# Performance work log

Hardware: AMD Instinct MI355X
Metric: run time of the kernel (lower is better)

Reference implementation:

```python
import jax, jax.numpy as jnp
import numpy as np

B, T, D, H, MLP, NI, OUT = 256, 2049, 64, 64, 128, 128, 10
L = D + D * (D - 1) // 2  # depth-2 logsignature channels = 2080


def _logsig_depth2(X, n_intervals):
    """Depth-2 log-signature of a piecewise-linear path over equal intervals.
    X: [B, T, D] with T = n_intervals*s + 1. Returns [B, n_intervals, L] where
    L = D + D(D-1)/2 (level-1 increments + strictly-upper-triangular Levy areas,
    the Lyndon-word basis signatory uses at depth 2)."""
    Bq, Tq, Dq = X.shape
    s = (Tq - 1) // n_intervals
    idx = np.arange(n_intervals)[:, None] * s + np.arange(s + 1)[None, :]
    seg = X[:, idx]                       # [B, n, s+1, D]
    inc = seg[:, :, -1] - seg[:, :, 0]    # level 1: [B, n, D]
    dlt = seg[:, :, 1:] - seg[:, :, :-1]  # per-step increments [B, n, s, D]
    cum = seg[:, :, :-1] - seg[:, :, :1]  # partial increments  [B, n, s, D]
    M = jnp.einsum('bnki,bnkj->bnij', cum, dlt)
    A = 0.5 * (M - jnp.swapaxes(M, -1, -2))  # Levy area [B, n, D, D]
    iu, ju = np.triu_indices(Dq, 1)
    return jnp.concatenate([inc, A[..., iu, ju]], axis=-1)  # [B, n, L]


def setup_inputs() -> dict:
    key = jax.random.key(0)
    ks = jax.random.split(key, 10)
    X = jax.random.normal(ks[0], (B, T, D), jnp.float32) * 0.05
    W_in = jax.random.normal(ks[1], (D, H), jnp.float32) / np.sqrt(D)
    b_in = jnp.zeros((H,), jnp.float32)
    W1 = jax.random.normal(ks[2], (H, MLP), jnp.float32) / np.sqrt(H)
    b1 = jnp.zeros((MLP,), jnp.float32)
    W2 = jax.random.normal(ks[3], (MLP, D * L), jnp.float32) / np.sqrt(MLP)
    b2 = jnp.zeros((D * L,), jnp.float32)
    W_out = jax.random.normal(ks[4], (H, OUT), jnp.float32) / np.sqrt(H)
    b_out = jnp.zeros((OUT,), jnp.float32)
    return {"X": X, "W_in": W_in, "b_in": b_in, "W1": W1, "b1": b1,
            "W2": W2, "b2": b2, "W_out": W_out, "b_out": b_out,
            "n_intervals": NI}


def reference(X, W_in, b_in, W1, b1, W2, b2, W_out, b_out, n_intervals):
    Bq, Tq, Dq = X.shape
    logsig = _logsig_depth2(X, n_intervals)        # [B, n, L]
    h0 = X[:, 0] @ W_in + b_in                     # initial_linear

    def vf(h):  # F.forward: MLP(h) -> [B, D, L]
        z = jnp.tanh(h @ W1 + b1)
        return (z @ W2 + b2).reshape(Bq, Dq, -1)

    def g(h, ls):  # f(h) contracted with logsig derivative
        return jnp.einsum('bdl,bl->bd', vf(h), ls)

    def rk4_step(h, ls):  # one RK4 step per interval, dt = 1
        k1 = g(h, ls)
        k2 = g(h + 0.5 * k1, ls)
        k3 = g(h + 0.5 * k2, ls)
        k4 = g(h + k3, ls)
        return h + (k1 + 2.0 * k2 + 2.0 * k3 + k4) / 6.0, None

    hT, _ = jax.lax.scan(rk4_step, h0, jnp.swapaxes(logsig, 0, 1))
    return hT @ W_out + b_out  # readout_linear: [B, OUT]
```

## Files before the change

### kernel.cpp

```cpp
#include <hip/hip_runtime.h>
#include <hip/hip_bf16.h>
#include <cstdint>
#include <cstddef>

#define B_SZ   256
#define T_SZ   2049
#define D_SZ   64
#define H_SZ   64
#define MLP_SZ 128
#define NI_SZ  128
#define SEG    16
#define KDIM   2080
#define KP     2112
#define OUT_SZ 10

#define NC     32
#define NCHUNK (NI_SZ / NC)
#define MROWS  (NC * B_SZ)
#define NB     8448
#define GSTR   8256
#define NT     (KP / 64)

typedef _Float16 f16x8 __attribute__((ext_vector_type(8)));
typedef float    f32x4 __attribute__((ext_vector_type(4)));

__device__ __forceinline__ float rlane(float v, int l) {
    return __uint_as_float(__builtin_amdgcn_readlane(__float_as_uint(v), l));
}

__global__ __launch_bounds__(256) void build_B(const float* __restrict__ W2,
                                               const float* __restrict__ b2,
                                               _Float16* __restrict__ Bm) {
    const int r = blockIdx.x, t = threadIdx.x;
    const float* src = nullptr;
    if (r < 8192) {
        const int d = r >> 7, m = r & 127;
        src = W2 + (size_t)m * (64 * KDIM) + (size_t)d * KDIM;
    } else if (r < 8256) {
        src = b2 + (size_t)(r - 8192) * KDIM;
    }
    _Float16* dst = Bm + (size_t)r * KP;
    for (int l = t; l < KP; l += 256)
        dst[l] = (src && l < KDIM) ? (_Float16)src[l] : (_Float16)0.0f;
}

__global__ void h0_kernel(const float* __restrict__ X, const float* __restrict__ W_in,
                          const float* __restrict__ b_in, float* __restrict__ h_state) {
    const int b = blockIdx.x, t = threadIdx.x;
    __shared__ float x0[D_SZ];
    if (t < D_SZ) x0[t] = X[(size_t)b * T_SZ * D_SZ + t];
    __syncthreads();
    float acc = b_in[t];
    for (int k = 0; k < D_SZ; ++k) acc += x0[k] * W_in[k * H_SZ + t];
    h_state[b * H_SZ + t] = acc;
}

__global__ __launch_bounds__(256) void logsig_kernel(const float* __restrict__ X,
                                                     _Float16* __restrict__ LS,
                                                     int n0) {
    const int b = blockIdx.x, sl = blockIdx.y, t = threadIdx.x;
    const int n = n0 + sl;
    __shared__ float seg[SEG + 1][D_SZ];
    __shared__ float cum[SEG][D_SZ];
    __shared__ float dlt[SEG][D_SZ];
    __shared__ float Mm[D_SZ][D_SZ + 1];

    const float* Xp = X + ((size_t)b * T_SZ + (size_t)n * SEG) * D_SZ;
    for (int i = t; i < (SEG + 1) * D_SZ / 4; i += 256)
        ((float4*)&seg[0][0])[i] = ((const float4*)Xp)[i];
    __syncthreads();
    for (int i = t; i < SEG * D_SZ; i += 256) {
        const int k = i >> 6, d = i & 63;
        cum[k][d] = seg[k][d] - seg[0][d];
        dlt[k][d] = seg[k + 1][d] - seg[k][d];
    }
    __syncthreads();

    const int ti = t >> 4, tj = t & 15;
    const int i0 = ti * 4, j0 = tj * 4;
    float m4[4][4] = {};
#pragma unroll
    for (int k = 0; k < SEG; ++k) {
        const float4 ci = *(const float4*)&cum[k][i0];
        const float4 dj = *(const float4*)&dlt[k][j0];
        const float* cip = (const float*)&ci;
        const float* djp = (const float*)&dj;
#pragma unroll
        for (int a = 0; a < 4; ++a)
#pragma unroll
            for (int c = 0; c < 4; ++c)
                m4[a][c] += cip[a] * djp[c];
    }
#pragma unroll
    for (int a = 0; a < 4; ++a)
#pragma unroll
        for (int c = 0; c < 4; ++c)
            Mm[i0 + a][j0 + c] = m4[a][c];
    __syncthreads();

    _Float16* out = LS + (size_t)(sl * B_SZ + b) * KP;
    if (t < D_SZ) out[t] = (_Float16)(seg[SEG][t] - seg[0][t]);
    if (t < KP - KDIM) out[KDIM + t] = (_Float16)0.0f;
    if (tj >= ti) {
#pragma unroll
        for (int a = 0; a < 4; ++a) {
            const int i = i0 + a;
#pragma unroll
            for (int c = 0; c < 4; ++c) {
                const int j = j0 + c;
                if (j > i) {
                    const int p = 63 * i - (i * (i - 1)) / 2 + (j - i - 1);
                    out[D_SZ + p] = (_Float16)(0.5f * (m4[a][c] - Mm[j][i]));
                }
            }
        }
    }
}

#define GLDS(SRC, DST) __builtin_amdgcn_global_load_lds(                        \
    (__attribute__((address_space(1))) void*)(SRC),                             \
    (__attribute__((address_space(3))) void*)(DST), 16, 0, 0)

#define STAGE(KT, KK, BUF) do {                                                 \
    const unsigned short* _sa = Asrc + (size_t)(KT) * 64 + (KK) * 32;           \
    const unsigned short* _sb = Bsrc + (size_t)(KT) * 64 + (KK) * 32;           \
    unsigned short* _d = ldst + (BUF) * 32768 + (KK) * 8192;                    \
    GLDS(_sa,                  _d);                                             \
    GLDS(_sa + (size_t)128*KP, _d + 4096);                                      \
    GLDS(_sb,                  _d + 16384);                                     \
    GLDS(_sb + (size_t)128*KP, _d + 20480);                                     \
} while (0)

#define BAR() do {                                                              \
    __builtin_amdgcn_sched_barrier(0);                                          \
    __builtin_amdgcn_s_barrier();                                               \
    __builtin_amdgcn_sched_barrier(0);                                          \
} while (0)

#define VMW_(N) asm volatile("s_waitcnt vmcnt(" #N ")" ::: "memory")
#define VMW(N) VMW_(N)

#define RD_A(S, PTR, KK, MB) do {                                               \
    a##S##0 = *(const f16x8*)((PTR) + (KK) * 8192 + ((MB) + 0) * 512);          \
    a##S##1 = *(const f16x8*)((PTR) + (KK) * 8192 + ((MB) + 1) * 512);          \
    a##S##2 = *(const f16x8*)((PTR) + (KK) * 8192 + ((MB) + 2) * 512);          \
    a##S##3 = *(const f16x8*)((PTR) + (KK) * 8192 + ((MB) + 3) * 512);          \
} while (0)

#define RD_B(S, PTR, KK) do {                                                   \
    b##S##0 = *(const f16x8*)((PTR) + (KK) * 8192 + 0 * 512);                   \
    b##S##1 = *(const f16x8*)((PTR) + (KK) * 8192 + 1 * 512);                   \
    b##S##2 = *(const f16x8*)((PTR) + (KK) * 8192 + 2 * 512);                   \
    b##S##3 = *(const f16x8*)((PTR) + (KK) * 8192 + 3 * 512);                   \
} while (0)

#define MFMA16(MB, AS, BS) do {                                                 \
    __builtin_amdgcn_s_setprio(1);                                              \
    acc[(MB)+0][0] = __builtin_amdgcn_mfma_f32_16x16x32_f16(a##AS##0, b##BS##0, acc[(MB)+0][0], 0, 0, 0); \
    acc[(MB)+0][1] = __builtin_amdgcn_mfma_f32_16x16x32_f16(a##AS##0, b##BS##1, acc[(MB)+0][1], 0, 0, 0); \
    acc[(MB)+1][0] = __builtin_amdgcn_mfma_f32_16x16x32_f16(a##AS##1, b##BS##0, acc[(MB)+1][0], 0, 0, 0); \
    acc[(MB)+1][1] = __builtin_amdgcn_mfma_f32_16x16x32_f16(a##AS##1, b##BS##1, acc[(MB)+1][1], 0, 0, 0); \
    acc[(MB)+0][2] = __builtin_amdgcn_mfma_f32_16x16x32_f16(a##AS##0, b##BS##2, acc[(MB)+0][2], 0, 0, 0); \
    acc[(MB)+0][3] = __builtin_amdgcn_mfma_f32_16x16x32_f16(a##AS##0, b##BS##3, acc[(MB)+0][3], 0, 0, 0); \
    acc[(MB)+1][2] = __builtin_amdgcn_mfma_f32_16x16x32_f16(a##AS##1, b##BS##2, acc[(MB)+1][2], 0, 0, 0); \
    acc[(MB)+1][3] = __builtin_amdgcn_mfma_f32_16x16x32_f16(a##AS##1, b##BS##3, acc[(MB)+1][3], 0, 0, 0); \
    acc[(MB)+2][0] = __builtin_amdgcn_mfma_f32_16x16x32_f16(a##AS##2, b##BS##0, acc[(MB)+2][0], 0, 0, 0); \
    acc[(MB)+2][1] = __builtin_amdgcn_mfma_f32_16x16x32_f16(a##AS##2, b##BS##1, acc[(MB)+2][1], 0, 0, 0); \
    acc[(MB)+3][0] = __builtin_amdgcn_mfma_f32_16x16x32_f16(a##AS##3, b##BS##0, acc[(MB)+3][0], 0, 0, 0); \
    acc[(MB)+3][1] = __builtin_amdgcn_mfma_f32_16x16x32_f16(a##AS##3, b##BS##1, acc[(MB)+3][1], 0, 0, 0); \
    acc[(MB)+2][2] = __builtin_amdgcn_mfma_f32_16x16x32_f16(a##AS##2, b##BS##2, acc[(MB)+2][2], 0, 0, 0); \
    acc[(MB)+2][3] = __builtin_amdgcn_mfma_f32_16x16x32_f16(a##AS##2, b##BS##3, acc[(MB)+2][3], 0, 0, 0); \
    acc[(MB)+3][2] = __builtin_amdgcn_mfma_f32_16x16x32_f16(a##AS##3, b##BS##2, acc[(MB)+3][2], 0, 0, 0); \
    acc[(MB)+3][3] = __builtin_amdgcn_mfma_f32_16x16x32_f16(a##AS##3, b##BS##3, acc[(MB)+3][3], 0, 0, 0); \
    __builtin_amdgcn_s_setprio(0);                                              \
} while (0)

#define TILE_BODY(TT, CUR, DOS1, DOS0, RDN, V1, V2) do {                        \
    const unsigned short* aC = aP + (CUR) * 32768;                              \
    const unsigned short* bC = bP + (CUR) * 32768;                              \
    const unsigned short* aN = aP + ((CUR) ^ 1) * 32768;                        \
    const unsigned short* bN = bP + ((CUR) ^ 1) * 32768;                        \
                                                                        \
    if (DOS1) { STAGE((TT) + 1, 1, (CUR) ^ 1); }                                \
    RD_A(1, aC, 0, 4);                                                          \
    MFMA16(0, 0, 0);                                                            \
    BAR();                                                                      \
                                                                        \
    RD_A(0, aC, 1, 0);                                                          \
    RD_B(1, bC, 1);                                                             \
    MFMA16(4, 1, 0);                                                            \
    VMW(V1); BAR();                                                             \
                                                                        \
    if (DOS0) { STAGE((TT) + 2, 0, (CUR)); }                                    \
    RD_A(1, aC, 1, 4);                                                          \
    MFMA16(0, 0, 1);                                                            \
    BAR();                                                                      \
                                                                        \
    if (RDN) { RD_A(0, aN, 0, 0); RD_B(0, bN, 0); }                             \
    MFMA16(4, 1, 1);                                                            \
    VMW(V2); BAR();                                                             \
} while (0)

__global__ __launch_bounds__(512, 2) void gemm256(const unsigned short* __restrict__ A,
                                                  const unsigned short* __restrict__ Bm,
                                                  _Float16* __restrict__ C) {
    __shared__ __align__(16) unsigned short lds[65536];
    const int t = threadIdx.x;

    const int wg = blockIdx.x;
    const int x  = (wg & 7) * 132 + (wg >> 3);
    const int bx = x / 33, by = x % 33;
    const int tileM = bx * 256, tileN = by * 256;

    const int q7s = (t >> 3) & 7;
    const int u   = (t & 7) ^ q7s;
    const int strow = ((t >> 3) << 1) + (u >> 2);
    const int stcol = (u & 3) << 3;
    const unsigned short* Asrc = A  + (size_t)(tileM + strow) * KP + stcol;
    const unsigned short* Bsrc = Bm + (size_t)(tileN + strow) * KP + stcol;
    unsigned short* ldst = lds + t * 8;

    const int lane = t & 63, w = t >> 6;
    const int wm = w >> 2, wn = w & 3;
    const int frow = lane & 15, j4 = lane >> 4;
    const int fr2 = frow >> 1;
    const int slot = (((frow & 1) << 2) | j4) ^ fr2;
    const unsigned short* aP = lds + wm * 4096 + fr2 * 64 + slot * 8;
    const unsigned short* bP = lds + 16384 + wn * 2048 + fr2 * 64 + slot * 8;

    f32x4 acc[8][4] = {};
    f16x8 a00, a01, a02, a03, a10, a11, a12, a13;
    f16x8 b00, b01, b02, b03, b10, b11, b12, b13;

    STAGE(0, 0, 0);
    STAGE(0, 1, 0);
    STAGE(1, 0, 1);
    VMW(4);
    BAR();
    RD_A(0, aP, 0, 0);
    RD_B(0, bP, 0);

    int cur = 0;
#pragma unroll 1
    for (int tt = 0; tt < NT - 2; ++tt) {
        TILE_BODY(tt, cur, 1, 1, 1, 4, 4);
        cur ^= 1;
    }
    TILE_BODY(NT - 2, cur, 1, 0, 1, 4, 0);
    cur ^= 1;
    TILE_BODY(NT - 1, cur, 0, 0, 0, 0, 0);

    const int erow = j4 << 2;
#pragma unroll
    for (int mi = 0; mi < 8; ++mi) {
        const int grow = tileM + wm * 128 + mi * 16 + erow;
#pragma unroll
        for (int ni = 0; ni < 4; ++ni) {
            const int gcol = tileN + wn * 64 + ni * 16 + frow;
            if (gcol < GSTR) {
                _Float16* cp = C + (size_t)grow * GSTR + gcol;
#pragma unroll
                for (int r = 0; r < 4; ++r)
                    cp[(size_t)r * GSTR] = (_Float16)acc[mi][ni][r];
            }
        }
    }
}

__global__ __launch_bounds__(256) void ode_chunk(const _Float16* __restrict__ G,
                                                 const float* __restrict__ W1,
                                                 const float* __restrict__ b1,
                                                 float* __restrict__ h_state) {
    const int b = blockIdx.x, t = threadIdx.x;
    const int lane = t & 63, w = t >> 6;
    const int j0 = w * 32 + (lane & 31);
    __shared__ float ysw[4][D_SZ];
    __shared__ float part[2][4][D_SZ];

    float w1c[D_SZ];
#pragma unroll
    for (int dd = 0; dd < D_SZ; ++dd) w1c[dd] = W1[dd * MLP_SZ + j0];
    const float b1v = b1[j0];

    float hsv = h_state[b * H_SZ + lane];
    ysw[w][lane] = hsv;
    float k_st[4] = {0.f, 0.f, 0.f, 0.f};

    f16x8 pr[4];
    _Float16 b2pre;
    {
        const _Float16* Gr = G + (size_t)b * GSTR;
        const f16x8* gp = (const f16x8*)(Gr + lane * 128 + w * 32);
#pragma unroll
        for (int v = 0; v < 4; ++v) pr[v] = gp[v];
        b2pre = Gr[8192 + lane];
    }

#pragma unroll 1
    for (int s = 0; s < NC; ++s) {
        float gcur[32];
#pragma unroll
        for (int v = 0; v < 4; ++v)
#pragma unroll
            for (int e = 0; e < 8; ++e) gcur[v * 8 + e] = (float)pr[v][e];
        const float b2cur = (float)b2pre;
        if (s + 1 < NC) {
            const _Float16* Gr = G + (size_t)((s + 1) * B_SZ + b) * GSTR;
            const f16x8* gp = (const f16x8*)(Gr + lane * 128 + w * 32);
#pragma unroll
            for (int v = 0; v < 4; ++v) pr[v] = gp[v];
            b2pre = Gr[8192 + lane];
        }

#pragma unroll
        for (int st = 0; st < 4; ++st) {
            float ax = 0.f, ay = 0.f, az = 0.f, aw = 0.f;
#pragma unroll
            for (int dd = 0; dd < D_SZ; dd += 4) {
                const float4 yv = *(const float4*)&ysw[w][dd];
                ax += yv.x * w1c[dd];
                ay += yv.y * w1c[dd + 1];
                az += yv.z * w1c[dd + 2];
                aw += yv.w * w1c[dd + 3];
            }
            const float xx = b1v + ((ax + ay) + (az + aw));
            const float ex = __expf(2.0f * xx);
            const float z = 1.0f - 2.0f / (ex + 1.0f);
            float s0 = 0.f, s1 = 0.f, s2 = 0.f, s3 = 0.f;
#pragma unroll
            for (int q = 0; q < 32; q += 4) {
                s0 += gcur[q]     * rlane(z, q);
                s1 += gcur[q + 1] * rlane(z, q + 1);
                s2 += gcur[q + 2] * rlane(z, q + 2);
                s3 += gcur[q + 3] * rlane(z, q + 3);
            }
            part[st & 1][w][lane] = (s0 + s1) + (s2 + s3);
            __syncthreads();
            const float kv = b2cur + part[st & 1][0][lane] + part[st & 1][1][lane]
                           + part[st & 1][2][lane] + part[st & 1][3][lane];
            k_st[st] = kv;
            if (st < 3) {
                float y = hsv;
                if (st == 0) y += 0.5f * kv;
                else if (st == 1) y += 0.5f * kv;
                else y += kv;
                ysw[w][lane] = y;
            }
        }
        hsv += (k_st[0] + 2.0f * k_st[1] + 2.0f * k_st[2] + k_st[3]) * (1.0f / 6.0f);
        ysw[w][lane] = hsv;
    }
    if (w == 0) h_state[b * H_SZ + lane] = hsv;
}

__global__ void out_kernel(const float* __restrict__ h_state, const float* __restrict__ W_out,
                           const float* __restrict__ b_out, float* __restrict__ out) {
    const int b = blockIdx.x, t = threadIdx.x;
    __shared__ float hh[H_SZ];
    hh[t] = h_state[b * H_SZ + t];
    __syncthreads();
    if (t < OUT_SZ) {
        float acc = b_out[t];
        for (int d = 0; d < H_SZ; ++d) acc += hh[d] * W_out[d * OUT_SZ + t];
        out[b * OUT_SZ + t] = acc;
    }
}

extern "C" void kernel_launch(void* const* d_in, const int* in_sizes, int n_in,
                              void* d_out, int out_size, void* d_ws, size_t ws_size,
                              hipStream_t stream) {
    (void)in_sizes; (void)n_in; (void)out_size; (void)ws_size;
    const float* X     = (const float*)d_in[0];
    const float* W_in  = (const float*)d_in[1];
    const float* b_in  = (const float*)d_in[2];
    const float* W1    = (const float*)d_in[3];
    const float* b1    = (const float*)d_in[4];
    const float* W2    = (const float*)d_in[5];
    const float* b2    = (const float*)d_in[6];
    const float* W_out = (const float*)d_in[7];
    const float* b_out = (const float*)d_in[8];
    float* out = (float*)d_out;

    char* ws = (char*)d_ws;
    size_t off = 0;
    auto take = [&](size_t bytes) { void* p = ws + off; off = (off + bytes + 255) & ~(size_t)255; return p; };
    _Float16* Bmat = (_Float16*)take((size_t)NB * KP * 2);
    _Float16* LSc  = (_Float16*)take((size_t)MROWS * KP * 2);
    _Float16* G    = (_Float16*)take((size_t)MROWS * GSTR * 2);
    float*    hst  = (float*)take((size_t)B_SZ * H_SZ * 4);

    build_B<<<NB, 256, 0, stream>>>(W2, b2, Bmat);
    h0_kernel<<<B_SZ, H_SZ, 0, stream>>>(X, W_in, b_in, hst);

    for (int c = 0; c < NCHUNK; ++c) {
        logsig_kernel<<<dim3(B_SZ, NC), 256, 0, stream>>>(X, LSc, c * NC);
        gemm256<<<dim3(1056), 512, 0, stream>>>(
            (const unsigned short*)LSc, (const unsigned short*)Bmat, G);
        ode_chunk<<<B_SZ, 256, 0, stream>>>(G, W1, b1, hst);
    }
    out_kernel<<<B_SZ, H_SZ, 0, stream>>>(hst, W_out, b_out, out);
}
```

Baseline: 1.975 ms.

## Split ragged GEMM column tail into dedicated narrow-tile blocks

```diff
diff --git a/kernel.cpp b/kernel.cpp
--- a/kernel.cpp
+++ b/kernel.cpp
@@ -137,7 +137,10 @@
     __builtin_amdgcn_sched_barrier(0);                                          \
 } while (0)
 
-#define VMW_(N) asm volatile("s_waitcnt vmcnt(" #N ")" ::: "memory")
+#define VMW_(N) do {                                                            \
+    __builtin_amdgcn_sched_barrier(0);                                          \
+    asm volatile("s_waitcnt vmcnt(" #N ")");                                    \
+} while (0)
 #define VMW(N) VMW_(N)
 
 #define RD_A(S, PTR, KK, MB) do {                                               \
@@ -206,10 +209,59 @@
                                                   _Float16* __restrict__ C) {
     __shared__ __align__(16) unsigned short lds[65536];
     const int t = threadIdx.x;
-
     const int wg = blockIdx.x;
-    const int x  = (wg & 7) * 132 + (wg >> 3);
-    const int bx = x / 33, by = x % 33;
+    const int lane = t & 63, w = t >> 6;
+    const int frow = lane & 15, j4 = lane >> 4;
+
+    if (wg < 32) {
+        unsigned short* sA = lds;
+        unsigned short* sB = lds + 8192;
+        const int tileM = wg * 256;
+        f32x4 acc[2][4] = {};
+        for (int k0 = 0; k0 < KP; k0 += 32) {
+            __syncthreads();
+#pragma unroll
+            for (int i = 0; i < 2; ++i) {
+                const int g = i * 8 + w;
+                const int row = g * 16 + (lane >> 2), kc = lane & 3;
+                GLDS(A + (size_t)(tileM + row) * KP + k0 + kc * 8,
+                     sA + g * 512 + lane * 8);
+            }
+            if (w < 4) {
+                const int row = w * 16 + (lane >> 2), kc = lane & 3;
+                GLDS(Bm + (size_t)(8192 + row) * KP + k0 + kc * 8,
+                     sB + w * 512 + lane * 8);
+            }
+            __syncthreads();
+            f16x8 bf[4];
+#pragma unroll
+            for (int ni = 0; ni < 4; ++ni)
+                bf[ni] = *(const f16x8*)(sB + (ni * 16 + frow) * 32 + j4 * 8);
+#pragma unroll
+            for (int mi = 0; mi < 2; ++mi) {
+                const f16x8 af = *(const f16x8*)(sA + (w * 32 + mi * 16 + frow) * 32 + j4 * 8);
+#pragma unroll
+                for (int ni = 0; ni < 4; ++ni)
+                    acc[mi][ni] = __builtin_amdgcn_mfma_f32_16x16x32_f16(af, bf[ni],
+                                                                         acc[mi][ni], 0, 0, 0);
+            }
+        }
+        const int erow = j4 << 2;
+#pragma unroll
+        for (int mi = 0; mi < 2; ++mi)
+#pragma unroll
+            for (int ni = 0; ni < 4; ++ni) {
+                const int grow = tileM + w * 32 + mi * 16 + erow;
+                const int gcol = 8192 + ni * 16 + frow;
+#pragma unroll
+                for (int r = 0; r < 4; ++r)
+                    C[(size_t)(grow + r) * GSTR + gcol] = (_Float16)acc[mi][ni][r];
+            }
+        return;
+    }
+
+    const int x  = ((wg - 32) & 7) * 128 + ((wg - 32) >> 3);
+    const int bx = x >> 5, by = x & 31;
     const int tileM = bx * 256, tileN = by * 256;
 
     const int q7s = (t >> 3) & 7;
@@ -220,9 +272,7 @@
     const unsigned short* Bsrc = Bm + (size_t)(tileN + strow) * KP + stcol;
     unsigned short* ldst = lds + t * 8;
 
-    const int lane = t & 63, w = t >> 6;
     const int wm = w >> 2, wn = w & 3;
-    const int frow = lane & 15, j4 = lane >> 4;
     const int fr2 = frow >> 1;
     const int slot = (((frow & 1) << 2) | j4) ^ fr2;
     const unsigned short* aP = lds + wm * 4096 + fr2 * 64 + slot * 8;
@@ -257,12 +307,10 @@
 #pragma unroll
         for (int ni = 0; ni < 4; ++ni) {
             const int gcol = tileN + wn * 64 + ni * 16 + frow;
-            if (gcol < GSTR) {
-                _Float16* cp = C + (size_t)grow * GSTR + gcol;
-#pragma unroll
-                for (int r = 0; r < 4; ++r)
-                    cp[(size_t)r * GSTR] = (_Float16)acc[mi][ni][r];
-            }
+            _Float16* cp = C + (size_t)grow * GSTR + gcol;
+#pragma unroll
+            for (int r = 0; r < 4; ++r)
+                cp[(size_t)r * GSTR] = (_Float16)acc[mi][ni][r];
         }
     }
 }
```

New measurement: 1.910 ms. -3.3%, faster.
